# Kernel optimization log

Hardware: AMD Instinct MI355X
Metric: run time of the kernel (lower is better)

Reference implementation:

```python
import jax, jax.numpy as jnp
import numpy as np


def setup_inputs() -> dict:
    key = jax.random.key(0)
    k1, k2, k3 = jax.random.split(key, 3)
    B, T, C = 4, 2048, 1024
    x = jax.random.normal(k1, (B, T, C), dtype=jnp.float32)
    # Linear weights stored as (in, out) so y = x @ W + b
    w_attn = jax.random.normal(k2, (C, 3 * C), dtype=jnp.float32) * (1.0 / np.sqrt(C))
    b_attn = jnp.zeros((3 * C,), dtype=jnp.float32)
    w_proj = jax.random.normal(k3, (C, C), dtype=jnp.float32) * (1.0 / np.sqrt(C))
    b_proj = jnp.zeros((C,), dtype=jnp.float32)
    return {"x": x, "w_attn": w_attn, "b_attn": b_attn, "w_proj": w_proj, "b_proj": b_proj}


def reference(x, w_attn, b_attn, w_proj, b_proj):
    B, T, C = x.shape
    n_head = 16
    hd = C // n_head  # head dim = 64
    qkv = x @ w_attn + b_attn  # [B, T, 3C]
    q, k, v = jnp.split(qkv, 3, axis=-1)
    # [B, H, T, hd]
    q = q.reshape(B, T, n_head, hd).transpose(0, 2, 1, 3)
    k = k.reshape(B, T, n_head, hd).transpose(0, 2, 1, 3)
    v = v.reshape(B, T, n_head, hd).transpose(0, 2, 1, 3)
    scale = 1.0 / np.sqrt(hd).astype(np.float32)
    att = jnp.einsum("bhqd,bhkd->bhqk", q, k) * scale  # [B, H, T, T]
    causal = jnp.tril(jnp.ones((T, T), dtype=bool))
    att = jnp.where(causal[None, None], att, jnp.float32(-jnp.inf))
    att = jax.nn.softmax(att, axis=-1)
    y = jnp.einsum("bhqk,bhkd->bhqd", att, v)  # [B, H, T, hd]
    y = y.transpose(0, 2, 1, 3).reshape(B, T, C)
    return y @ w_proj + b_proj
```

## Files before the change

kernel.cpp:

```cpp
#include <hip/hip_runtime.h>

typedef __attribute__((ext_vector_type(8))) short short8;
typedef __attribute__((ext_vector_type(4))) float f32x4;
typedef __attribute__((ext_vector_type(16))) float f32x16;
typedef unsigned short u16;
typedef unsigned int u32;

__device__ __forceinline__ float bf2f(u16 u) {
    union { u32 i; float f; } x;
    x.i = ((u32)u) << 16;
    return x.f;
}

__device__ __forceinline__ u16 f2bf(float f) {
    union { float f; u32 i; } x;
    x.f = f;
    u32 r = x.i + 0x7fffu + ((x.i >> 16) & 1u);
    return (u16)(r >> 16);
}

__device__ __forceinline__ u32 cvt_pk_bf16(float lo, float hi) {
    u32 d;
    asm("v_cvt_pk_bf16_f32 %0, %1, %2" : "=v"(d) : "v"(lo), "v"(hi));
    return d;
}

__device__ __forceinline__ void gload_lds16(const u16* g, u16* l) {
    __builtin_amdgcn_global_load_lds(
        (const __attribute__((address_space(1))) void*)g,
        (__attribute__((address_space(3))) void*)l, 16, 0, 0);
}

__device__ __forceinline__ void pswap(u32& a, u32& b) {
#if __has_builtin(__builtin_amdgcn_permlane32_swap)
    auto r = __builtin_amdgcn_permlane32_swap(a, b, false, false);
    a = r[0];
    b = r[1];
#else
    const int l = (int)(threadIdx.x & 63);
    const u32 ax = __shfl(a, l ^ 32);
    const u32 bx = __shfl(b, l ^ 32);
    a = (l < 32) ? a : bx;
    b = (l < 32) ? ax : b;
#endif
}

#if __has_builtin(__builtin_amdgcn_exp2f)
#define EXP2F(x) __builtin_amdgcn_exp2f(x)
#else
#define EXP2F(x) exp2f(x)
#endif

#define K_SCALE 0.18033688f

__global__ __launch_bounds__(256) void prep_kernel(const float* __restrict__ x,
                                                   u16* __restrict__ xb,
                                                   const float* __restrict__ w_attn,
                                                   u16* __restrict__ wTa) {
    __shared__ float tile[32][33];
    const int tid = threadIdx.x;
    if (blockIdx.x < 4096) {
        const long i = ((long)blockIdx.x * 256 + tid) * 8;
        f32x4 v0 = *(const f32x4*)(x + i);
        f32x4 v1 = *(const f32x4*)(x + i + 4);
        short8 o;
#pragma unroll
        for (int j = 0; j < 4; ++j) o[j] = (short)f2bf(v0[j]);
#pragma unroll
        for (int j = 0; j < 4; ++j) o[4 + j] = (short)f2bf(v1[j]);
        *(short8*)(xb + i) = o;
    } else {
        const int bid = blockIdx.x - 4096;
        const int nb = (bid % 96) * 32, kb = (bid / 96) * 32;
        const int tx = tid & 31, ty = tid >> 5;
#pragma unroll
        for (int i = 0; i < 32; i += 8)
            tile[ty + i][tx] = w_attn[(long)(kb + ty + i) * 3072 + nb + tx];
        __syncthreads();
#pragma unroll
        for (int i = 0; i < 32; i += 8)
            wTa[(long)(nb + ty + i) * 1024 + kb + tx] = f2bf(tile[tx][ty + i]);
    }
}

__global__ __launch_bounds__(256) void transpose_v(const u16* __restrict__ qkv,
                                                   u16* __restrict__ vT) {
    __shared__ u16 tile[32][33];
    const int tb = blockIdx.x * 32;
    const int db = blockIdx.y * 32;
    const int bh = blockIdx.z;
    const int b = bh >> 4, h = bh & 15;
    const int tx = threadIdx.x, ty = threadIdx.y;
#pragma unroll
    for (int i = 0; i < 32; i += 8)
        tile[ty + i][tx] = qkv[((long)b * 2048 + tb + ty + i) * 3072 + 2048 + h * 64 + db + tx];
    __syncthreads();
#pragma unroll
    for (int i = 0; i < 32; i += 8)
        vT[((long)bh * 64 + db + ty + i) * 2048 + tb + tx] = tile[tx][ty + i];
}

__global__ __launch_bounds__(256) void transpose_wp(const float* __restrict__ w,
                                                    u16* __restrict__ dst) {
    __shared__ float tile[32][33];
    const int nb = blockIdx.x * 32, kb = blockIdx.y * 32;
    const int tx = threadIdx.x & 31, ty = threadIdx.x >> 5;
#pragma unroll
    for (int i = 0; i < 32; i += 8)
        tile[ty + i][tx] = w[(long)(kb + ty + i) * 1024 + nb + tx];
    __syncthreads();
#pragma unroll
    for (int i = 0; i < 32; i += 8)
        dst[(long)(nb + ty + i) * 3072 + kb + tx] = f2bf(tile[tx][ty + i]);
}

#define G_STAGE(KOFF, SLOT)                                                   \
    gload_lds16(Ag + (KOFF), &As[(SLOT)*4096 + wbase]);                       \
    gload_lds16(Ag + (KOFF) + (long)16 * lda, &As[(SLOT)*4096 + wbase + 512]);\
    gload_lds16(Bg + (KOFF), &Bs[(SLOT)*4096 + wbase]);                       \
    gload_lds16(Bg + (KOFF) + (long)16 * ldbv, &Bs[(SLOT)*4096 + wbase + 512]);

#define G_COMPUTE(SLOT)                                                       \
    {                                                                         \
        short8 af[4], bf[4];                                                  \
        _Pragma("unroll")                                                     \
        for (int mt = 0; mt < 4; ++mt)                                        \
            af[mt] = *(const short8*)&As[(SLOT)*4096 + (wm + mt*16 + L)*32 + quad*8]; \
        _Pragma("unroll")                                                     \
        for (int nt = 0; nt < 4; ++nt)                                        \
            bf[nt] = *(const short8*)&Bs[(SLOT)*4096 + (wn + nt*16 + L)*32 + quad*8]; \
        _Pragma("unroll")                                                     \
        for (int mt = 0; mt < 4; ++mt)                                        \
            _Pragma("unroll")                                                 \
            for (int nt = 0; nt < 4; ++nt)                                    \
                acc[mt][nt] = __builtin_amdgcn_mfma_f32_16x16x32_bf16(        \
                    af[mt], bf[nt], acc[mt][nt], 0, 0, 0);                    \
    }

#define G_RING_LOOP                                                           \
    G_STAGE(0, 0);                                                            \
    G_STAGE(32, 1);                                                           \
    int slot = 0, s2 = 2;                                                     \
    for (int kb = 0; kb + 64 < K; kb += 32) {                                 \
        asm volatile("s_waitcnt vmcnt(4)" ::: "memory");                      \
        __builtin_amdgcn_s_barrier();                                         \
        G_STAGE(kb + 64, s2);                                                 \
        G_COMPUTE(slot);                                                      \
        slot = (slot + 1 == 3) ? 0 : slot + 1;                                \
        s2 = (s2 + 1 == 3) ? 0 : s2 + 1;                                      \
    }                                                                         \
    asm volatile("s_waitcnt vmcnt(4)" ::: "memory");                          \
    __builtin_amdgcn_s_barrier();                                             \
    G_COMPUTE(slot);                                                          \
    slot = (slot + 1 == 3) ? 0 : slot + 1;                                    \
    asm volatile("s_waitcnt vmcnt(0)" ::: "memory");                          \
    __builtin_amdgcn_s_barrier();                                             \
    G_COMPUTE(slot);

__global__ __launch_bounds__(256, 3) void gemm_bf16_bt(
    const u16* __restrict__ A, int lda, const u16* __restrict__ BT,
    const float* __restrict__ bias, u16* __restrict__ C,
    int M, int N, int K) {
    __shared__ __align__(16) u16 As[3 * 128 * 32];
    __shared__ __align__(16) u16 Bs[3 * 128 * 32];
    const int tid = threadIdx.x;
    const int wv = tid >> 6, lane = tid & 63, quad = lane >> 4, L = lane & 15;
    const int wm = (wv >> 1) * 64, wn = (wv & 1) * 64;
    const long m0 = (long)blockIdx.y * 128;
    const long n0 = (long)blockIdx.x * 128;

    const u16* Ag = A + (m0 + wv * 32 + (lane >> 2)) * (long)lda + (lane & 3) * 8;
    const u16* Bg = BT + (n0 + wv * 32 + (lane >> 2)) * (long)K + (lane & 3) * 8;
    const long ldbv = K;
    const int wbase = wv * 1024;

    f32x4 zero4 = {0.f, 0.f, 0.f, 0.f};
    f32x4 acc[4][4];
#pragma unroll
    for (int i = 0; i < 4; ++i)
#pragma unroll
        for (int j = 0; j < 4; ++j) acc[i][j] = zero4;

    G_RING_LOOP

#pragma unroll
    for (int nt = 0; nt < 4; ++nt) {
        const long col = n0 + wn + nt * 16 + L;
        const float bv = bias[col];
        const float scl = (col >= 1024 && col < 2048) ? K_SCALE : 1.0f;
#pragma unroll
        for (int mt = 0; mt < 4; ++mt)
#pragma unroll
            for (int r = 0; r < 4; ++r) {
                const long row = m0 + wm + mt * 16 + quad * 4 + r;
                C[row * N + col] = f2bf((acc[mt][nt][r] + bv) * scl);
            }
    }
}

__global__ __launch_bounds__(256, 3) void gemm_bt2(
    const u16* __restrict__ A, int lda, const u16* __restrict__ BT, int ldb,
    const float* __restrict__ bias, float* __restrict__ C,
    int M, int N, int K) {
    __shared__ __align__(16) u16 As[3 * 128 * 32];
    __shared__ __align__(16) u16 Bs[3 * 128 * 32];
    const int tid = threadIdx.x;
    const int wv = tid >> 6, lane = tid & 63, quad = lane >> 4, L = lane & 15;
    const int wm = (wv >> 1) * 64, wn = (wv & 1) * 64;
    const long m0 = (long)blockIdx.y * 128;
    const long n0 = (long)blockIdx.x * 128;

    const u16* Ag = A + (m0 + wv * 32 + (lane >> 2)) * (long)lda + (lane & 3) * 8;
    const u16* Bg = BT + (n0 + wv * 32 + (lane >> 2)) * (long)ldb + (lane & 3) * 8;
    const long ldbv = ldb;
    const int wbase = wv * 1024;

    f32x4 zero4 = {0.f, 0.f, 0.f, 0.f};
    f32x4 acc[4][4];
#pragma unroll
    for (int i = 0; i < 4; ++i)
#pragma unroll
        for (int j = 0; j < 4; ++j) acc[i][j] = zero4;

    G_RING_LOOP

#pragma unroll
    for (int nt = 0; nt < 4; ++nt) {
        const long col = n0 + wn + nt * 16 + L;
        const float bv = bias[col];
#pragma unroll
        for (int mt = 0; mt < 4; ++mt)
#pragma unroll
            for (int r = 0; r < 4; ++r) {
                const long row = m0 + wm + mt * 16 + quad * 4 + r;
                C[row * N + col] = acc[mt][nt][r] + bv;
            }
    }
}

#define AT_T 2048

__global__ __launch_bounds__(256) void attn_kernel(u16* __restrict__ qkv,
                                                   const u16* __restrict__ vT) {
    __shared__ u16 Kt[2][64 * 72];
    __shared__ u16 Vt[2][64 * 72];
    const int tid = threadIdx.x;
    const int wv = tid >> 6, lane = tid & 63;
    const int hi = lane >> 5, cc = lane & 31;
    const int bh = blockIdx.x;
    const int b = bh >> 4, h = bh & 15;
    const long rowbase = (long)b * AT_T;
    const long cbase = (long)h * 64;

    const int srow = tid >> 3, sc = tid & 7;
    const u16* Kg = qkv + (rowbase + srow) * 3072 + 1024 + cbase + sc * 8;
    const u16* Vg = vT + ((long)bh * 64 + srow) * 2048 + sc * 8;
    const int kLo = srow * 72 + sc * 8, kHi = (srow + 32) * 72 + sc * 8;

    short8 ones;
#pragma unroll
    for (int j = 0; j < 8; ++j) ones[j] = (cc == 0) ? (short)0x3F80 : (short)0;

    f32x16 z16;
#pragma unroll
    for (int r = 0; r < 16; ++r) z16[r] = 0.f;

    for (int pass = 0; pass < 2; ++pass) {
        const int qt = (pass == 0) ? (15 - (int)blockIdx.y) : (int)blockIdx.y;
        const int qw = qt * 128 + wv * 32;
        const int nkb = 2 * qt + 2;

        short8 qf[4];
#pragma unroll
        for (int ks = 0; ks < 4; ++ks)
            qf[ks] = *(const short8*)&qkv[(rowbase + qw + cc) * 3072 + cbase + ks * 16 + hi * 8];

        f32x16 accO0, accO1, accL;
#pragma unroll
        for (int r = 0; r < 16; ++r) { accO0[r] = 0.f; accO1[r] = 0.f; accL[r] = 0.f; }

        {
            *(short8*)&Kt[0][kLo] = *(const short8*)Kg;
            *(short8*)&Kt[0][kHi] = *(const short8*)(Kg + (long)32 * 3072);
            *(short8*)&Vt[0][kLo] = *(const short8*)Vg;
            *(short8*)&Vt[0][kHi] = *(const short8*)(Vg + (long)32 * 2048);
        }
        __syncthreads();

        int p = 0;
        for (int kb = 0; kb < nkb; ++kb) {
            const int k0 = kb * 64;
            const bool more = (kb + 1) < nkb;
            short8 kn0, kn1, vn0, vn1;
            if (more) {
                kn0 = *(const short8*)(Kg + (long)(k0 + 64) * 3072);
                kn1 = *(const short8*)(Kg + (long)(k0 + 96) * 3072);
                vn0 = *(const short8*)(Vg + k0 + 64);
                vn1 = *(const short8*)(Vg + (long)32 * 2048 + k0 + 64);
            }

#pragma unroll
            for (int hh = 0; hh < 2; ++hh) {
                const int kh = k0 + 32 * hh;
                if (kh <= qw) {
                    f32x16 s;
                    __builtin_amdgcn_s_setprio(1);
                    {
                        short8 kf = *(const short8*)&Kt[p][(32 * hh + cc) * 72 + hi * 8];
                        s = __builtin_amdgcn_mfma_f32_32x32x16_bf16(kf, qf[0], z16, 0, 0, 0);
                    }
#pragma unroll
                    for (int ks = 1; ks < 4; ++ks) {
                        short8 kf = *(const short8*)&Kt[p][(32 * hh + cc) * 72 + ks * 16 + hi * 8];
                        s = __builtin_amdgcn_mfma_f32_32x32x16_bf16(kf, qf[ks], s, 0, 0, 0);
                    }
                    __builtin_amdgcn_s_setprio(0);
                    float pe[16];
                    if (kh == qw) {
#pragma unroll
                        for (int r = 0; r < 16; ++r) {
                            const int key = (r & 3) + 8 * (r >> 2) + 4 * hi;
                            const float e = EXP2F(s[r]);
                            pe[r] = (key <= cc) ? e : 0.f;
                        }
                    } else {
#pragma unroll
                        for (int r = 0; r < 16; ++r) pe[r] = EXP2F(s[r]);
                    }

                    short8 pa[2];
#pragma unroll
                    for (int ks = 0; ks < 2; ++ks) {
                        u32 wA = cvt_pk_bf16(pe[8 * ks + 0], pe[8 * ks + 1]);
                        u32 wB = cvt_pk_bf16(pe[8 * ks + 2], pe[8 * ks + 3]);
                        u32 wC = cvt_pk_bf16(pe[8 * ks + 4], pe[8 * ks + 5]);
                        u32 wD = cvt_pk_bf16(pe[8 * ks + 6], pe[8 * ks + 7]);
                        pswap(wA, wC);
                        pswap(wB, wD);
                        union { u32 d[4]; short8 v; } u;
                        u.d[0] = wA; u.d[1] = wB; u.d[2] = wC; u.d[3] = wD;
                        pa[ks] = u.v;
                    }

                    __builtin_amdgcn_s_setprio(1);
                    accL = __builtin_amdgcn_mfma_f32_32x32x16_bf16(pa[0], ones, accL, 0, 0, 0);
                    accL = __builtin_amdgcn_mfma_f32_32x32x16_bf16(pa[1], ones, accL, 0, 0, 0);
#pragma unroll
                    for (int ks = 0; ks < 2; ++ks) {
                        short8 vf0 = *(const short8*)&Vt[p][cc * 72 + 32 * hh + ks * 16 + hi * 8];
                        short8 vf1 = *(const short8*)&Vt[p][(32 + cc) * 72 + 32 * hh + ks * 16 + hi * 8];
                        accO0 = __builtin_amdgcn_mfma_f32_32x32x16_bf16(pa[ks], vf0, accO0, 0, 0, 0);
                        accO1 = __builtin_amdgcn_mfma_f32_32x32x16_bf16(pa[ks], vf1, accO1, 0, 0, 0);
                    }
                    __builtin_amdgcn_s_setprio(0);
                }
            }

            if (more) {
                *(short8*)&Kt[p ^ 1][kLo] = kn0;
                *(short8*)&Kt[p ^ 1][kHi] = kn1;
                *(short8*)&Vt[p ^ 1][kLo] = vn0;
                *(short8*)&Vt[p ^ 1][kHi] = vn1;
            }
            __syncthreads();
            p ^= 1;
        }

#pragma unroll
        for (int r = 0; r < 16; ++r) {
            const float l = __shfl(accL[r], lane & 32);
            const float inv = 1.f / l;
            const int q = (r & 3) + 8 * (r >> 2) + 4 * hi;
            const long orow = (rowbase + qw + q) * 3072 + cbase;
            qkv[orow + cc] = f2bf(accO0[r] * inv);
            qkv[orow + 32 + cc] = f2bf(accO1[r] * inv);
        }
    }
}

extern "C" void kernel_launch(void* const* d_in, const int* in_sizes, int n_in,
                              void* d_out, int out_size, void* d_ws, size_t ws_size,
                              hipStream_t stream) {
    const float* x      = (const float*)d_in[0];
    const float* w_attn = (const float*)d_in[1];
    const float* b_attn = (const float*)d_in[2];
    const float* w_proj = (const float*)d_in[3];
    const float* b_proj = (const float*)d_in[4];
    float* out = (float*)d_out;

    u16* qkv = (u16*)d_ws;
    u16* xb  = (u16*)d_out;
    u16* wTa = (u16*)((char*)d_out + 16777216);
    u16* vT  = (u16*)d_out;
    u16* wTp = qkv + 2048;

    prep_kernel<<<4096 + 3072, 256, 0, stream>>>(x, xb, w_attn, wTa);
    gemm_bf16_bt<<<dim3(3072 / 128, 8192 / 128), 256, 0, stream>>>(
        xb, 1024, wTa, b_attn, qkv, 8192, 3072, 1024);
    transpose_v<<<dim3(64, 2, 64), dim3(32, 8), 0, stream>>>(qkv, vT);
    transpose_wp<<<dim3(32, 32), 256, 0, stream>>>(w_proj, wTp);
    attn_kernel<<<dim3(64, 8), 256, 0, stream>>>(qkv, vT);
    gemm_bt2<<<dim3(1024 / 128, 8192 / 128), 256, 0, stream>>>(
        qkv, 3072, wTp, 3072, b_proj, out, 8192, 1024, 1024);
}
```

Baseline: 252.1 us.

## Switch GEMMs to 32x32x16 MFMA and add XCD-aware block swizzle

The QKV and projection GEMM kernels now compute each wave's 64x64 tile with 2x2 32x32x16 bf16 MFMAs instead of 4x4 16x16x32 MFMAs. The LDS fragment reads and the epilogue row mapping change to match the new accumulator layout. A block-id swizzle spreads consecutive workgroups across the 8 XCDs to improve L2 locality. The larger MFMA shape needs fewer instructions and fragment loads per tile, but the LDS read pattern changes and bank conflicts may differ.

```diff
diff --git a/kernel.cpp b/kernel.cpp
--- a/kernel.cpp
+++ b/kernel.cpp
@@ -122,19 +122,28 @@
 
 #define G_COMPUTE(SLOT)                                                       \
     {                                                                         \
-        short8 af[4], bf[4];                                                  \
+        short8 af[2][2], bf[2][2];                                            \
         _Pragma("unroll")                                                     \
-        for (int mt = 0; mt < 4; ++mt)                                        \
-            af[mt] = *(const short8*)&As[(SLOT)*4096 + (wm + mt*16 + L)*32 + quad*8]; \
+        for (int mt = 0; mt < 2; ++mt)                                        \
+            _Pragma("unroll")                                                 \
+            for (int kh = 0; kh < 2; ++kh)                                    \
+                af[mt][kh] = *(const short8*)&As[(SLOT)*4096 +                \
+                    (wm + mt*32 + cc)*32 + kh*16 + hi*8];                     \
         _Pragma("unroll")                                                     \
-        for (int nt = 0; nt < 4; ++nt)                                        \
-            bf[nt] = *(const short8*)&Bs[(SLOT)*4096 + (wn + nt*16 + L)*32 + quad*8]; \
+        for (int nt = 0; nt < 2; ++nt)                                        \
+            _Pragma("unroll")                                                 \
+            for (int kh = 0; kh < 2; ++kh)                                    \
+                bf[nt][kh] = *(const short8*)&Bs[(SLOT)*4096 +                \
+                    (wn + nt*32 + cc)*32 + kh*16 + hi*8];                     \
         _Pragma("unroll")                                                     \
-        for (int mt = 0; mt < 4; ++mt)                                        \
+        for (int mt = 0; mt < 2; ++mt)                                        \
             _Pragma("unroll")                                                 \
-            for (int nt = 0; nt < 4; ++nt)                                    \
-                acc[mt][nt] = __builtin_amdgcn_mfma_f32_16x16x32_bf16(        \
-                    af[mt], bf[nt], acc[mt][nt], 0, 0, 0);                    \
+            for (int nt = 0; nt < 2; ++nt) {                                  \
+                acc[mt][nt] = __builtin_amdgcn_mfma_f32_32x32x16_bf16(        \
+                    af[mt][0], bf[nt][0], acc[mt][nt], 0, 0, 0);              \
+                acc[mt][nt] = __builtin_amdgcn_mfma_f32_32x32x16_bf16(        \
+                    af[mt][1], bf[nt][1], acc[mt][nt], 0, 0, 0);              \
+            }                                                                 \
     }
 
 #define G_RING_LOOP                                                           \
@@ -157,6 +166,12 @@
     __builtin_amdgcn_s_barrier();                                             \
     G_COMPUTE(slot);
 
+#define G_BID_SWZ                                                             \
+    const int nwg = gridDim.x * gridDim.y;                                    \
+    const int bid0 = blockIdx.y * gridDim.x + blockIdx.x;                     \
+    const int sb = (bid0 & 7) * (nwg >> 3) + (bid0 >> 3);                     \
+    const int bx = sb % gridDim.x, by = sb / gridDim.x;
+
 __global__ __launch_bounds__(256, 3) void gemm_bf16_bt(
     const u16* __restrict__ A, int lda, const u16* __restrict__ BT,
     const float* __restrict__ bias, u16* __restrict__ C,
@@ -164,35 +179,38 @@
     __shared__ __align__(16) u16 As[3 * 128 * 32];
     __shared__ __align__(16) u16 Bs[3 * 128 * 32];
     const int tid = threadIdx.x;
-    const int wv = tid >> 6, lane = tid & 63, quad = lane >> 4, L = lane & 15;
+    const int wv = tid >> 6, lane = tid & 63;
+    const int cc = lane & 31, hi = lane >> 5;
     const int wm = (wv >> 1) * 64, wn = (wv & 1) * 64;
-    const long m0 = (long)blockIdx.y * 128;
-    const long n0 = (long)blockIdx.x * 128;
+    G_BID_SWZ
+    const long m0 = (long)by * 128;
+    const long n0 = (long)bx * 128;
 
     const u16* Ag = A + (m0 + wv * 32 + (lane >> 2)) * (long)lda + (lane & 3) * 8;
     const u16* Bg = BT + (n0 + wv * 32 + (lane >> 2)) * (long)K + (lane & 3) * 8;
     const long ldbv = K;
     const int wbase = wv * 1024;
 
-    f32x4 zero4 = {0.f, 0.f, 0.f, 0.f};
-    f32x4 acc[4][4];
-#pragma unroll
-    for (int i = 0; i < 4; ++i)
-#pragma unroll
-        for (int j = 0; j < 4; ++j) acc[i][j] = zero4;
+    f32x16 acc[2][2];
+#pragma unroll
+    for (int i = 0; i < 2; ++i)
+#pragma unroll
+        for (int j = 0; j < 2; ++j)
+#pragma unroll
+            for (int r = 0; r < 16; ++r) acc[i][j][r] = 0.f;
 
     G_RING_LOOP
 
 #pragma unroll
-    for (int nt = 0; nt < 4; ++nt) {
-        const long col = n0 + wn + nt * 16 + L;
+    for (int nt = 0; nt < 2; ++nt) {
+        const long col = n0 + wn + nt * 32 + cc;
         const float bv = bias[col];
         const float scl = (col >= 1024 && col < 2048) ? K_SCALE : 1.0f;
 #pragma unroll
-        for (int mt = 0; mt < 4; ++mt)
-#pragma unroll
-            for (int r = 0; r < 4; ++r) {
-                const long row = m0 + wm + mt * 16 + quad * 4 + r;
+        for (int mt = 0; mt < 2; ++mt)
+#pragma unroll
+            for (int r = 0; r < 16; ++r) {
+                const long row = m0 + wm + mt * 32 + (r & 3) + 8 * (r >> 2) + 4 * hi;
                 C[row * N + col] = f2bf((acc[mt][nt][r] + bv) * scl);
             }
     }
@@ -205,34 +223,37 @@
     __shared__ __align__(16) u16 As[3 * 128 * 32];
     __shared__ __align__(16) u16 Bs[3 * 128 * 32];
     const int tid = threadIdx.x;
-    const int wv = tid >> 6, lane = tid & 63, quad = lane >> 4, L = lane & 15;
+    const int wv = tid >> 6, lane = tid & 63;
+    const int cc = lane & 31, hi = lane >> 5;
     const int wm = (wv >> 1) * 64, wn = (wv & 1) * 64;
-    const long m0 = (long)blockIdx.y * 128;
-    const long n0 = (long)blockIdx.x * 128;
+    G_BID_SWZ
+    const long m0 = (long)by * 128;
+    const long n0 = (long)bx * 128;
 
     const u16* Ag = A + (m0 + wv * 32 + (lane >> 2)) * (long)lda + (lane & 3) * 8;
     const u16* Bg = BT + (n0 + wv * 32 + (lane >> 2)) * (long)ldb + (lane & 3) * 8;
     const long ldbv = ldb;
     const int wbase = wv * 1024;
 
-    f32x4 zero4 = {0.f, 0.f, 0.f, 0.f};
-    f32x4 acc[4][4];
-#pragma unroll
-    for (int i = 0; i < 4; ++i)
-#pragma unroll
-        for (int j = 0; j < 4; ++j) acc[i][j] = zero4;
+    f32x16 acc[2][2];
+#pragma unroll
+    for (int i = 0; i < 2; ++i)
+#pragma unroll
+        for (int j = 0; j < 2; ++j)
+#pragma unroll
+            for (int r = 0; r < 16; ++r) acc[i][j][r] = 0.f;
 
     G_RING_LOOP
 
 #pragma unroll
-    for (int nt = 0; nt < 4; ++nt) {
-        const long col = n0 + wn + nt * 16 + L;
+    for (int nt = 0; nt < 2; ++nt) {
+        const long col = n0 + wn + nt * 32 + cc;
         const float bv = bias[col];
 #pragma unroll
-        for (int mt = 0; mt < 4; ++mt)
-#pragma unroll
-            for (int r = 0; r < 4; ++r) {
-                const long row = m0 + wm + mt * 16 + quad * 4 + r;
+        for (int mt = 0; mt < 2; ++mt)
+#pragma unroll
+            for (int r = 0; r < 16; ++r) {
+                const long row = m0 + wm + mt * 32 + (r & 3) + 8 * (r >> 2) + 4 * hi;
                 C[row * N + col] = acc[mt][nt][r] + bv;
             }
     }
```

New measurement: 264.9 us. 1.05x slower.

## Fuse V transpose into QKV GEMM epilogue and swizzle GEMM block order

Applied to the files above, without the earlier changes.

When the workspace is large enough, the QKV GEMM writes the V columns directly in transposed layout by staging the tile through LDS, so the separate transpose_v kernel is skipped. Both GEMMs also remap block ids so consecutive workgroups are spread in an interleaved order, aiming for better cache locality. This saves a kernel launch and an extra read/write pass over V, at the cost of an extra LDS round-trip and barriers in the V-tile epilogue. The fused path depends on the workspace size at runtime.

```diff
diff --git a/kernel.cpp b/kernel.cpp
--- a/kernel.cpp
+++ b/kernel.cpp
@@ -1,6 +1,7 @@
 #include <hip/hip_runtime.h>
 
 typedef __attribute__((ext_vector_type(8))) short short8;
+typedef __attribute__((ext_vector_type(4))) short short4v;
 typedef __attribute__((ext_vector_type(4))) float f32x4;
 typedef __attribute__((ext_vector_type(16))) float f32x16;
 typedef unsigned short u16;
@@ -157,17 +158,25 @@
     __builtin_amdgcn_s_barrier();                                             \
     G_COMPUTE(slot);
 
+#define G_BID_SWZ                                                             \
+    const int nwg = gridDim.x * gridDim.y;                                    \
+    const int bid0 = blockIdx.y * gridDim.x + blockIdx.x;                     \
+    const int sb = (bid0 & 7) * (nwg >> 3) + (bid0 >> 3);                     \
+    const int bx = sb % gridDim.x, by = sb / gridDim.x;
+
 __global__ __launch_bounds__(256, 3) void gemm_bf16_bt(
     const u16* __restrict__ A, int lda, const u16* __restrict__ BT,
     const float* __restrict__ bias, u16* __restrict__ C,
-    int M, int N, int K) {
-    __shared__ __align__(16) u16 As[3 * 128 * 32];
-    __shared__ __align__(16) u16 Bs[3 * 128 * 32];
+    u16* __restrict__ vTd, int M, int N, int K) {
+    __shared__ __align__(16) u16 RingLDS[2 * 3 * 4096];
+    u16* const As = RingLDS;
+    u16* const Bs = RingLDS + 3 * 4096;
     const int tid = threadIdx.x;
     const int wv = tid >> 6, lane = tid & 63, quad = lane >> 4, L = lane & 15;
     const int wm = (wv >> 1) * 64, wn = (wv & 1) * 64;
-    const long m0 = (long)blockIdx.y * 128;
-    const long n0 = (long)blockIdx.x * 128;
+    G_BID_SWZ
+    const long m0 = (long)by * 128;
+    const long n0 = (long)bx * 128;
 
     const u16* Ag = A + (m0 + wv * 32 + (lane >> 2)) * (long)lda + (lane & 3) * 8;
     const u16* Bg = BT + (n0 + wv * 32 + (lane >> 2)) * (long)K + (lane & 3) * 8;
@@ -183,18 +192,46 @@
 
     G_RING_LOOP
 
-#pragma unroll
-    for (int nt = 0; nt < 4; ++nt) {
-        const long col = n0 + wn + nt * 16 + L;
-        const float bv = bias[col];
-        const float scl = (col >= 1024 && col < 2048) ? K_SCALE : 1.0f;
-#pragma unroll
-        for (int mt = 0; mt < 4; ++mt)
-#pragma unroll
-            for (int r = 0; r < 4; ++r) {
-                const long row = m0 + wm + mt * 16 + quad * 4 + r;
-                C[row * N + col] = f2bf((acc[mt][nt][r] + bv) * scl);
+    if (vTd != nullptr && n0 >= 2048) {
+        __syncthreads();
+        u16* Tl = RingLDS;
+#pragma unroll
+        for (int nt = 0; nt < 4; ++nt) {
+            const int cl = wn + nt * 16 + L;
+            const float bv = bias[n0 + cl];
+#pragma unroll
+            for (int mt = 0; mt < 4; ++mt) {
+                short4v pv;
+#pragma unroll
+                for (int r = 0; r < 4; ++r) pv[r] = (short)f2bf(acc[mt][nt][r] + bv);
+                *(short4v*)&Tl[cl * 136 + wm + mt * 16 + quad * 4] = pv;
             }
+        }
+        __syncthreads();
+        const int j = tid >> 1, half = tid & 1;
+        const int colg = (int)(n0 - 2048) + j;
+        const int h = colg >> 6, d = colg & 63;
+        const long bq = m0 >> 11;
+        const long t0 = (m0 & 2047) + half * 64;
+        u16* dst = vTd + (((bq * 16 + h) * 64 + d) * 2048) + t0;
+        const u16* src = &Tl[j * 136 + half * 64];
+#pragma unroll
+        for (int q8 = 0; q8 < 8; ++q8)
+            *(short8*)(dst + q8 * 8) = *(const short8*)(src + q8 * 8);
+    } else {
+#pragma unroll
+        for (int nt = 0; nt < 4; ++nt) {
+            const long col = n0 + wn + nt * 16 + L;
+            const float bv = bias[col];
+            const float scl = (col >= 1024 && col < 2048) ? K_SCALE : 1.0f;
+#pragma unroll
+            for (int mt = 0; mt < 4; ++mt)
+#pragma unroll
+                for (int r = 0; r < 4; ++r) {
+                    const long row = m0 + wm + mt * 16 + quad * 4 + r;
+                    C[row * N + col] = f2bf((acc[mt][nt][r] + bv) * scl);
+                }
+        }
     }
 }
 
@@ -202,13 +239,15 @@
     const u16* __restrict__ A, int lda, const u16* __restrict__ BT, int ldb,
     const float* __restrict__ bias, float* __restrict__ C,
     int M, int N, int K) {
-    __shared__ __align__(16) u16 As[3 * 128 * 32];
-    __shared__ __align__(16) u16 Bs[3 * 128 * 32];
+    __shared__ __align__(16) u16 RingLDS[2 * 3 * 4096];
+    u16* const As = RingLDS;
+    u16* const Bs = RingLDS + 3 * 4096;
     const int tid = threadIdx.x;
     const int wv = tid >> 6, lane = tid & 63, quad = lane >> 4, L = lane & 15;
     const int wm = (wv >> 1) * 64, wn = (wv & 1) * 64;
-    const long m0 = (long)blockIdx.y * 128;
-    const long n0 = (long)blockIdx.x * 128;
+    G_BID_SWZ
+    const long m0 = (long)by * 128;
+    const long n0 = (long)bx * 128;
 
     const u16* Ag = A + (m0 + wv * 32 + (lane >> 2)) * (long)lda + (lane & 3) * 8;
     const u16* Bg = BT + (n0 + wv * 32 + (lane >> 2)) * (long)ldb + (lane & 3) * 8;
@@ -391,13 +430,17 @@
     u16* qkv = (u16*)d_ws;
     u16* xb  = (u16*)d_out;
     u16* wTa = (u16*)((char*)d_out + 16777216);
-    u16* vT  = (u16*)d_out;
     u16* wTp = qkv + 2048;
+
+    const bool fused_v = (ws_size >= (size_t)50331648 + 16777216);
+    u16* vT = fused_v ? qkv + (size_t)8192 * 3072
+                      : (u16*)d_out;
 
     prep_kernel<<<4096 + 3072, 256, 0, stream>>>(x, xb, w_attn, wTa);
     gemm_bf16_bt<<<dim3(3072 / 128, 8192 / 128), 256, 0, stream>>>(
-        xb, 1024, wTa, b_attn, qkv, 8192, 3072, 1024);
-    transpose_v<<<dim3(64, 2, 64), dim3(32, 8), 0, stream>>>(qkv, vT);
+        xb, 1024, wTa, b_attn, qkv, fused_v ? vT : nullptr, 8192, 3072, 1024);
+    if (!fused_v)
+        transpose_v<<<dim3(64, 2, 64), dim3(32, 8), 0, stream>>>(qkv, vT);
     transpose_wp<<<dim3(32, 32), 256, 0, stream>>>(w_proj, wTp);
     attn_kernel<<<dim3(64, 8), 256, 0, stream>>>(qkv, vT);
     gemm_bt2<<<dim3(1024 / 128, 8192 / 128), 256, 0, stream>>>(
```

After: 241.7 us. -4.1%, faster.
